# Optimization experiments

Hardware: AMD Instinct MI355X
Metric: run time of the kernel (lower is better)

## Reference

```python
import jax, jax.numpy as jnp
import numpy as np
import math


def _build_lookup(S):
    # Vectorized port of build_hierarchical_index_lookup_table (static, numpy).
    L = int(math.log2(S))
    total = 2 * S - 1
    max_valid = total - 2  # root is never a neighbor
    idx = np.full((S, L), -1, dtype=np.int32)
    cmask = np.zeros((S, L), dtype=bool)
    n = np.arange(S, dtype=np.int64)
    for lvl in range(L):
        if lvl == 0:
            nn = n ^ 1
            pair = n
        else:
            pair = n // 2 + S
            nn = pair ^ 1
        valid = nn <= max_valid
        idx[:, lvl] = np.where(valid, nn.astype(np.int32), idx[:, lvl])
        cmask[:, lvl] = np.where(valid, (pair < nn) & valid, cmask[:, lvl])
        n = nn
    return jnp.asarray(idx), jnp.asarray(cmask)


def _tree_kv(k, v, levels, scale):
    # Build parent nodes bottom-up. Parent K is the mean of its two children;
    # parent V is refined by the fused parent-self attention (build_parent_nodes):
    # 3-way softmax over [self, child0, child1] with eps 1e-9 in the denominator.
    K_parts, V_parts = [k], [v]
    Kc, Vc = k, v
    for _ in range(levels):
        Kc0, Kc1 = Kc[:, 0::2], Kc[:, 1::2]
        Vc0, Vc1 = Vc[:, 0::2], Vc[:, 1::2]
        Kp = 0.5 * (Kc0 + Kc1)
        Vp = 0.5 * (Vc0 + Vc1)
        s_self = jnp.einsum('bphd,bphd->bph', Kp, Kp) * scale
        s0 = jnp.einsum('bphd,bphd->bph', Kp, Kc0) * scale
        s1 = jnp.einsum('bphd,bphd->bph', Kp, Kc1) * scale
        m = jnp.maximum(s_self, jnp.maximum(s0, s1))
        e_self = jnp.exp(s_self - m)
        e0 = jnp.exp(s0 - m)
        e1 = jnp.exp(s1 - m)
        denom = e_self + e0 + e1 + 1e-9
        Vp = (e_self[..., None] * Vp + e0[..., None] * Vc0 + e1[..., None] * Vc1) / denom[..., None]
        K_parts.append(Kp)
        V_parts.append(Vp)
        Kc, Vc = Kp, Vp
    # Full tree: leaves first, then each parent level -> [B, 2S-1, H, D]
    return jnp.concatenate(K_parts, axis=1), jnp.concatenate(V_parts, axis=1)


def setup_inputs() -> dict:
    key = jax.random.key(0)
    kq, kk, kv = jax.random.split(key, 3)
    B, S, H, D = 4, 4096, 8, 64
    q = jax.random.normal(kq, (B, S, H, D), dtype=jnp.float32)
    k = jax.random.normal(kk, (B, S, H, D), dtype=jnp.float32)
    v = jax.random.normal(kv, (B, S, H, D), dtype=jnp.float32)
    return {'q': q, 'k': k, 'v': v}


def reference(q, k, v):
    B, S, H, D = q.shape
    L = int(math.log2(S))
    scale = 1.0 / math.sqrt(D)
    idx, cmask = _build_lookup(S)          # [S, L] int32, [S, L] bool
    Kf, Vf = _tree_kv(k, v, L, scale)      # [B, 2S-1, H, D]
    kc = Kf[:, idx]                        # [B, S, L, H, D] tree-indexed gather
    vc = Vf[:, idx]
    s_self = jnp.einsum('bshd,bshd->bsh', q, k) * scale
    s_cross = jnp.einsum('bshd,bslhd->bshl', q, kc) * scale
    s_cross = jnp.where(cmask[None, :, None, :], -jnp.inf, s_cross)
    m = jnp.maximum(s_self, jnp.max(s_cross, axis=-1))  # online-softmax max
    e_self = jnp.exp(s_self - m)
    e_cross = jnp.exp(s_cross - m[..., None])
    denom = e_self + jnp.sum(e_cross, axis=-1)
    out = (e_self[..., None] * v + jnp.einsum('bshl,bslhd->bshd', e_cross, vc)) / denom[..., None]
    return out
```

## Files before the change

kernel.cpp:

```cpp
#include <hip/hip_runtime.h>


#define S 4096
#define H 8
#define D 64
#define B 4
#define NBH 32
#define NHI 254
#define SCALE 0.125f
#define ROWF 68

__device__ inline float red16(float x) {
    x += __shfl_xor(x, 1);
    x += __shfl_xor(x, 2);
    x += __shfl_xor(x, 4);
    x += __shfl_xor(x, 8);
    return x;
}

__device__ inline float dot4(const float4 a, const float4 b) {
    return a.x * b.x + a.y * b.y + a.z * b.z + a.w * b.w;
}

__device__ inline float4 shfl_xor4(const float4 x, int m) {
    float4 r;
    r.x = __shfl_xor(x.x, m);
    r.y = __shfl_xor(x.y, m);
    r.z = __shfl_xor(x.z, m);
    r.w = __shfl_xor(x.w, m);
    return r;
}

__device__ inline float4 sel4(bool c, const float4 a, const float4 b) {
    float4 r;
    r.x = c ? a.x : b.x;
    r.y = c ? a.y : b.y;
    r.z = c ? a.z : b.z;
    r.w = c ? a.w : b.w;
    return r;
}

__device__ inline void combine(const float4 k0, const float4 k1,
                               const float4 v0, const float4 v1,
                               float4& kp, float4& vp) {
    kp.x = 0.5f * (k0.x + k1.x);
    kp.y = 0.5f * (k0.y + k1.y);
    kp.z = 0.5f * (k0.z + k1.z);
    kp.w = 0.5f * (k0.w + k1.w);
    float pss = red16(dot4(kp, kp)) * SCALE;
    float p0  = red16(dot4(kp, k0)) * SCALE;
    float p1  = red16(dot4(kp, k1)) * SCALE;
    float m  = fmaxf(pss, fmaxf(p0, p1));
    float es = __expf(pss - m), e0 = __expf(p0 - m), e1 = __expf(p1 - m);
    float inv = 1.0f / (es + e0 + e1 + 1e-9f);
    float h = 0.5f * es;
    vp.x = ((h + e0) * v0.x + (h + e1) * v1.x) * inv;
    vp.y = ((h + e0) * v0.y + (h + e1) * v1.y) * inv;
    vp.z = ((h + e0) * v0.z + (h + e1) * v1.z) * inv;
    vp.w = ((h + e0) * v0.w + (h + e1) * v1.w) * inv;
}

__global__ __launch_bounds__(256, 6) void chunk5(
    const float* __restrict__ k, const float* __restrict__ v,
    float* __restrict__ khi, float* __restrict__ vhi)
{
    __shared__ float l4k[4 * ROWF], l4v[4 * ROWF];
    const int t = threadIdx.x;
    const int sub = t & 15;
    const int pg = t >> 4;
    const int blk = blockIdx.x;
    const int pair = blk & 63;
    const int bh = blk >> 6;
    const int b = bh >> 3, h = bh & 7;
    const int csel = pg >> 3;
    const int jg = pg & 7;
    const int c = pair * 2 + csel;

    const int s0 = c * 32 + 4 * jg;
    const size_t a0 = ((((size_t)b * S + s0) * H + h) * D) + sub * 4;
    float4 kA = *(const float4*)(k + a0);
    float4 kB = *(const float4*)(k + a0 + H * D);
    float4 kC = *(const float4*)(k + a0 + 2 * H * D);
    float4 kD = *(const float4*)(k + a0 + 3 * H * D);
    float4 vA = *(const float4*)(v + a0);
    float4 vB = *(const float4*)(v + a0 + H * D);
    float4 vC = *(const float4*)(v + a0 + 2 * H * D);
    float4 vD = *(const float4*)(v + a0 + 3 * H * D);

    float4 k1a, v1a, k1b, v1b, k2, v2;
    combine(kA, kB, vA, vB, k1a, v1a);
    combine(kC, kD, vC, vD, k1b, v1b);
    combine(k1a, k1b, v1a, v1b, k2, v2);

    float4 p2k = shfl_xor4(k2, 16), p2v = shfl_xor4(v2, 16);
    float4 k3, v3;
    combine(sel4(jg & 1, p2k, k2), sel4(jg & 1, k2, p2k),
            sel4(jg & 1, p2v, v2), sel4(jg & 1, v2, p2v), k3, v3);

    float4 p3k = shfl_xor4(k3, 32), p3v = shfl_xor4(v3, 32);
    float4 k4, v4;
    combine(sel4(jg & 2, p3k, k3), sel4(jg & 2, k3, p3k),
            sel4(jg & 2, p3v, v3), sel4(jg & 2, v3, p3v), k4, v4);

    if ((jg & 3) == 0) {
        int row = csel * 2 + (jg >> 2);
        *(float4*)(l4k + row * ROWF + sub * 4) = k4;
        *(float4*)(l4v + row * ROWF + sub * 4) = v4;
    }
    __syncthreads();
    if (jg == 0) {
        int r0 = csel * 2, r1 = csel * 2 + 1;
        float4 ka4 = *(const float4*)(l4k + r0 * ROWF + sub * 4);
        float4 kb4 = *(const float4*)(l4k + r1 * ROWF + sub * 4);
        float4 va4 = *(const float4*)(l4v + r0 * ROWF + sub * 4);
        float4 vb4 = *(const float4*)(l4v + r1 * ROWF + sub * 4);
        float4 kp, vp;
        combine(ka4, kb4, va4, vb4, kp, vp);
        size_t g = ((size_t)bh * NHI + c) * 64 + sub * 4;
        *(float4*)(khi + g) = kp;
        *(float4*)(vhi + g) = vp;
    }
}

__global__ __launch_bounds__(256) void build_hi_half(
    float* __restrict__ khi, float* __restrict__ vhi)
{
    __shared__ float lk[64 * ROWF], lv[64 * ROWF];
    const int t = threadIdx.x;
    const int sub = t & 15;
    const int pg = t >> 4;
    const int bh = blockIdx.x >> 1;
    const int half = blockIdx.x & 1;
    size_t base = (size_t)bh * NHI * 64;
    const int rootO = half * 64;

    for (int i = t; i < 1024; i += 256) {
        int row = i >> 4, s16 = i & 15;
        *(float4*)(lk + row * ROWF + s16 * 4) =
            *(const float4*)(khi + base + (size_t)(rootO + row) * 64 + s16 * 4);
        *(float4*)(lv + row * ROWF + s16 * 4) =
            *(const float4*)(vhi + base + (size_t)(rootO + row) * 64 + s16 * 4);
    }
    __syncthreads();

#pragma unroll
    for (int tt = 1; tt <= 6; ++tt) {
        int nodes = 64 >> tt;
        int off = 256 - (256 >> tt);
        for (int j = pg; j < nodes; j += 16) {
            int r0 = (2 * j) << (tt - 1);
            int r1 = (2 * j + 1) << (tt - 1);
            float4 k0 = *(const float4*)(lk + r0 * ROWF + sub * 4);
            float4 k1 = *(const float4*)(lk + r1 * ROWF + sub * 4);
            float4 v0 = *(const float4*)(lv + r0 * ROWF + sub * 4);
            float4 v1 = *(const float4*)(lv + r1 * ROWF + sub * 4);
            float4 kp, vp;
            combine(k0, k1, v0, v1, kp, vp);
            *(float4*)(lk + (j << tt) * ROWF + sub * 4) = kp;
            *(float4*)(lv + (j << tt) * ROWF + sub * 4) = vp;
            size_t g = base + (size_t)(off + half * nodes + j) * 64 + sub * 4;
            *(float4*)(khi + g) = kp;
            *(float4*)(vhi + g) = vp;
        }
        __syncthreads();
    }
}

__global__ __launch_bounds__(256, 8) void attn32(
    const float* __restrict__ q, const float* __restrict__ k,
    const float* __restrict__ v,
    const float* __restrict__ khi, const float* __restrict__ vhi,
    float* __restrict__ out)
{
    __shared__ float tk[30 * ROWF], tv[30 * ROWF];
    __shared__ float pk[7 * ROWF], pv[7 * ROWF];
    const int t = threadIdx.x;
    const int sub = t & 15;
    const int pg = t >> 4;
    const int blk = blockIdx.x;
    const int c32 = blk & 127;
    const int bh = blk >> 7;
    const int b = bh >> 3, h = bh & 7;

    {
        int pl = (pg < 7) ? pg : pg - 8;
        if (pl >= 0 && pl < 7 && pg != 7 && pg != 15) {
            if ((c32 >> pl) & 1) {
                int off = 256 - (256 >> pl);
                int node = off + ((c32 >> pl) ^ 1);
                size_t a = ((size_t)bh * NHI + node) * 64 + sub * 4;
                if (pg < 7) *(float4*)(pk + pl * ROWF + sub * 4) = *(const float4*)(khi + a);
                else        *(float4*)(pv + pl * ROWF + sub * 4) = *(const float4*)(vhi + a);
            }
        }
    }

    const int s0 = c32 * 32 + 2 * pg;
    const size_t a0 = ((((size_t)b * S + s0) * H + h) * D) + sub * 4;
    const float4 k0 = *(const float4*)(k + a0);
    const float4 k1 = *(const float4*)(k + a0 + H * D);
    const float4 v0 = *(const float4*)(v + a0);
    const float4 v1 = *(const float4*)(v + a0 + H * D);
    const float4 q0 = *(const float4*)(q + a0);
    const float4 q1 = *(const float4*)(q + a0 + H * D);

    {
        float4 kp, vp;
        combine(k0, k1, v0, v1, kp, vp);
        *(float4*)(tk + pg * ROWF + sub * 4) = kp;
        *(float4*)(tv + pg * ROWF + sub * 4) = vp;
    }
    __syncthreads();

    if (pg < 8) {
        float4 ka = *(const float4*)(tk + (2 * pg) * ROWF + sub * 4);
        float4 kb = *(const float4*)(tk + (2 * pg + 1) * ROWF + sub * 4);
        float4 va = *(const float4*)(tv + (2 * pg) * ROWF + sub * 4);
        float4 vb = *(const float4*)(tv + (2 * pg + 1) * ROWF + sub * 4);
        float4 kp, vp;
        combine(ka, kb, va, vb, kp, vp);
        *(float4*)(tk + (16 + pg) * ROWF + sub * 4) = kp;
        *(float4*)(tv + (16 + pg) * ROWF + sub * 4) = vp;
    }
    __syncthreads();

    if (pg < 4) {
        float4 ka = *(const float4*)(tk + (16 + 2 * pg) * ROWF + sub * 4);
        float4 kb = *(const float4*)(tk + (16 + 2 * pg + 1) * ROWF + sub * 4);
        float4 va = *(const float4*)(tv + (16 + 2 * pg) * ROWF + sub * 4);
        float4 vb = *(const float4*)(tv + (16 + 2 * pg + 1) * ROWF + sub * 4);
        float4 kp, vp;
        combine(ka, kb, va, vb, kp, vp);
        *(float4*)(tk + (24 + pg) * ROWF + sub * 4) = kp;
        *(float4*)(tv + (24 + pg) * ROWF + sub * 4) = vp;
    }
    __syncthreads();

    if (pg < 2) {
        float4 ka = *(const float4*)(tk + (24 + 2 * pg) * ROWF + sub * 4);
        float4 kb = *(const float4*)(tk + (24 + 2 * pg + 1) * ROWF + sub * 4);
        float4 va = *(const float4*)(tv + (24 + 2 * pg) * ROWF + sub * 4);
        float4 vb = *(const float4*)(tv + (24 + 2 * pg + 1) * ROWF + sub * 4);
        float4 kp, vp;
        combine(ka, kb, va, vb, kp, vp);
        *(float4*)(tk + (28 + pg) * ROWF + sub * 4) = kp;
        *(float4*)(tv + (28 + pg) * ROWF + sub * 4) = vp;
    }
    __syncthreads();

#pragma unroll
    for (int r = 0; r < 2; ++r) {
        const int s = s0 + r;
        const float4 q4 = r ? q1 : q0;
        const float4 k4 = r ? k1 : k0;
        const float4 v4 = r ? v1 : v0;

        float ss = red16(dot4(q4, k4)) * SCALE;

        float sc[12];
        if (r) sc[0] = red16(dot4(q4, k0)) * SCALE;
        else   sc[0] = -1e38f;
#pragma unroll
        for (int l = 1; l <= 4; ++l) {
            if ((s >> l) & 1) {
                int base = 32 - (32 >> (l - 1));
                int loc = base + (((s >> l) ^ 1) - (c32 << (5 - l)));
                float4 kc = *(const float4*)(tk + loc * ROWF + sub * 4);
                sc[l] = red16(dot4(q4, kc)) * SCALE;
            } else sc[l] = -1e38f;
        }
#pragma unroll
        for (int l = 5; l <= 11; ++l) {
            if ((c32 >> (l - 5)) & 1) {
                float4 kc = *(const float4*)(pk + (l - 5) * ROWF + sub * 4);
                sc[l] = red16(dot4(q4, kc)) * SCALE;
            } else sc[l] = -1e38f;
        }

        float m = ss;
#pragma unroll
        for (int l = 0; l < 12; ++l) m = fmaxf(m, sc[l]);

        float es = __expf(ss - m);
        float denom = es;
        float4 acc;
        acc.x = es * v4.x; acc.y = es * v4.y;
        acc.z = es * v4.z; acc.w = es * v4.w;

        if (r) {
            float e = __expf(sc[0] - m);
            denom += e;
            acc.x += e * v0.x; acc.y += e * v0.y;
            acc.z += e * v0.z; acc.w += e * v0.w;
        }
#pragma unroll
        for (int l = 1; l <= 4; ++l) {
            if ((s >> l) & 1) {
                int base = 32 - (32 >> (l - 1));
                int loc = base + (((s >> l) ^ 1) - (c32 << (5 - l)));
                float4 vc = *(const float4*)(tv + loc * ROWF + sub * 4);
                float e = __expf(sc[l] - m);
                denom += e;
                acc.x += e * vc.x; acc.y += e * vc.y;
                acc.z += e * vc.z; acc.w += e * vc.w;
            }
        }
#pragma unroll
        for (int l = 5; l <= 11; ++l) {
            if ((c32 >> (l - 5)) & 1) {
                float4 vc = *(const float4*)(pv + (l - 5) * ROWF + sub * 4);
                float e = __expf(sc[l] - m);
                denom += e;
                acc.x += e * vc.x; acc.y += e * vc.y;
                acc.z += e * vc.z; acc.w += e * vc.w;
            }
        }
        float inv = 1.0f / denom;
        float4 o;
        o.x = acc.x * inv; o.y = acc.y * inv;
        o.z = acc.z * inv; o.w = acc.w * inv;
        *(float4*)(out + a0 + r * H * D) = o;
    }
}

extern "C" void kernel_launch(void* const* d_in, const int* in_sizes, int n_in,
                              void* d_out, int out_size, void* d_ws, size_t ws_size,
                              hipStream_t stream) {
    const float* q = (const float*)d_in[0];
    const float* k = (const float*)d_in[1];
    const float* v = (const float*)d_in[2];
    float* outp = (float*)d_out;
    float* khi = (float*)d_ws;
    float* vhi = khi + (size_t)NBH * NHI * D;

    hipLaunchKernelGGL(chunk5, dim3(NBH * 64), dim3(256), 0, stream,
                       k, v, khi, vhi);
    hipLaunchKernelGGL(build_hi_half, dim3(NBH * 2), dim3(256), 0, stream,
                       khi, vhi);
    hipLaunchKernelGGL(attn32, dim3(NBH * 128), dim3(256), 0, stream,
                       q, k, v, khi, vhi, outp);
}
```

Measured before the change: 157.4 us.

## Batch score reductions with a transposing butterfly across 16 lanes

Rewrites the attention phase so each lane accumulates partial dot products for all 16 candidate scores into a register array, then reduces them with a transposing butterfly. After it, each lane holds one full score, where before every score needed its own 4-step shuffle reduction. Max, exp and denominator are then computed lane-parallel, and weights are broadcast with shuffles for the V accumulation. Leaf-level dot products are interleaved with the tree-build phases, and launch bounds drop from 8 to 6 waves to allow more registers. The risk is higher register pressure from the two 16-float arrays and lower occupancy.

New measurement: 149.7 us. 1.05x faster.

```diff
diff --git a/kernel.cpp b/kernel.cpp
--- a/kernel.cpp
+++ b/kernel.cpp
@@ -38,6 +38,37 @@
     r.z = c ? a.z : b.z;
     r.w = c ? a.w : b.w;
     return r;
+}
+
+__device__ inline float bfly16(float* p, int sub) {
+    int b = (sub >> 3) & 1;
+#pragma unroll
+    for (int j = 0; j < 8; ++j) {
+        float mine = b ? p[j + 8] : p[j];
+        float send = b ? p[j] : p[j + 8];
+        p[j] = mine + __shfl_xor(send, 8);
+    }
+    b = (sub >> 2) & 1;
+#pragma unroll
+    for (int j = 0; j < 4; ++j) {
+        float mine = b ? p[j + 4] : p[j];
+        float send = b ? p[j] : p[j + 4];
+        p[j] = mine + __shfl_xor(send, 4);
+    }
+    b = (sub >> 1) & 1;
+#pragma unroll
+    for (int j = 0; j < 2; ++j) {
+        float mine = b ? p[j + 2] : p[j];
+        float send = b ? p[j] : p[j + 2];
+        p[j] = mine + __shfl_xor(send, 2);
+    }
+    b = sub & 1;
+    {
+        float mine = b ? p[1] : p[0];
+        float send = b ? p[0] : p[1];
+        p[0] = mine + __shfl_xor(send, 1);
+    }
+    return p[0];
 }
 
 __device__ inline void combine(const float4 k0, const float4 k1,
@@ -166,7 +197,7 @@
     }
 }
 
-__global__ __launch_bounds__(256, 8) void attn32(
+__global__ __launch_bounds__(256, 6) void attn32(
     const float* __restrict__ q, const float* __restrict__ k,
     const float* __restrict__ v,
     const float* __restrict__ khi, const float* __restrict__ vhi,
@@ -204,6 +235,13 @@
     const float4 q0 = *(const float4*)(q + a0);
     const float4 q1 = *(const float4*)(q + a0 + H * D);
 
+    float p0[16], p1[16];
+#pragma unroll
+    for (int j = 0; j < 16; ++j) { p0[j] = 0.0f; p1[j] = 0.0f; }
+    p0[0] = dot4(q0, k0);
+    p1[0] = dot4(q1, k1);
+    p1[1] = dot4(q1, k0);
+
     {
         float4 kp, vp;
         combine(k0, k1, v0, v1, kp, vp);
@@ -212,6 +250,11 @@
     }
     __syncthreads();
 
+    if (pg & 1) {
+        float4 kc = *(const float4*)(tk + (pg ^ 1) * ROWF + sub * 4);
+        p0[2] = dot4(q0, kc);
+        p1[2] = dot4(q1, kc);
+    }
     if (pg < 8) {
         float4 ka = *(const float4*)(tk + (2 * pg) * ROWF + sub * 4);
         float4 kb = *(const float4*)(tk + (2 * pg + 1) * ROWF + sub * 4);
@@ -224,6 +267,11 @@
     }
     __syncthreads();
 
+    if ((pg >> 1) & 1) {
+        float4 kc = *(const float4*)(tk + (16 + ((pg >> 1) ^ 1)) * ROWF + sub * 4);
+        p0[3] = dot4(q0, kc);
+        p1[3] = dot4(q1, kc);
+    }
     if (pg < 4) {
         float4 ka = *(const float4*)(tk + (16 + 2 * pg) * ROWF + sub * 4);
         float4 kb = *(const float4*)(tk + (16 + 2 * pg + 1) * ROWF + sub * 4);
@@ -236,6 +284,11 @@
     }
     __syncthreads();
 
+    if ((pg >> 2) & 1) {
+        float4 kc = *(const float4*)(tk + (24 + ((pg >> 2) ^ 1)) * ROWF + sub * 4);
+        p0[4] = dot4(q0, kc);
+        p1[4] = dot4(q1, kc);
+    }
     if (pg < 2) {
         float4 ka = *(const float4*)(tk + (24 + 2 * pg) * ROWF + sub * 4);
         float4 kb = *(const float4*)(tk + (24 + 2 * pg + 1) * ROWF + sub * 4);
@@ -248,79 +301,91 @@
     }
     __syncthreads();
 
-#pragma unroll
-    for (int r = 0; r < 2; ++r) {
-        const int s = s0 + r;
-        const float4 q4 = r ? q1 : q0;
-        const float4 k4 = r ? k1 : k0;
-        const float4 v4 = r ? v1 : v0;
-
-        float ss = red16(dot4(q4, k4)) * SCALE;
-
-        float sc[12];
-        if (r) sc[0] = red16(dot4(q4, k0)) * SCALE;
-        else   sc[0] = -1e38f;
-#pragma unroll
-        for (int l = 1; l <= 4; ++l) {
-            if ((s >> l) & 1) {
-                int base = 32 - (32 >> (l - 1));
-                int loc = base + (((s >> l) ^ 1) - (c32 << (5 - l)));
-                float4 kc = *(const float4*)(tk + loc * ROWF + sub * 4);
-                sc[l] = red16(dot4(q4, kc)) * SCALE;
-            } else sc[l] = -1e38f;
+    if ((pg >> 3) & 1) {
+        float4 kc = *(const float4*)(tk + (28 + ((pg >> 3) ^ 1)) * ROWF + sub * 4);
+        p0[5] = dot4(q0, kc);
+        p1[5] = dot4(q1, kc);
+    }
+#pragma unroll
+    for (int l = 5; l <= 11; ++l) {
+        if ((c32 >> (l - 5)) & 1) {
+            float4 kc = *(const float4*)(pk + (l - 5) * ROWF + sub * 4);
+            p0[l + 1] = dot4(q0, kc);
+            p1[l + 1] = dot4(q1, kc);
         }
-#pragma unroll
-        for (int l = 5; l <= 11; ++l) {
-            if ((c32 >> (l - 5)) & 1) {
-                float4 kc = *(const float4*)(pk + (l - 5) * ROWF + sub * 4);
-                sc[l] = red16(dot4(q4, kc)) * SCALE;
-            } else sc[l] = -1e38f;
+    }
+
+    float sc0 = bfly16(p0, sub) * SCALE;
+    float sc1 = bfly16(p1, sub) * SCALE;
+
+    const bool vcom =
+        (sub == 0) ||
+        (sub >= 2 && sub <= 5 && ((pg >> (sub - 2)) & 1)) ||
+        (sub >= 6 && sub <= 12 && ((c32 >> (sub - 6)) & 1));
+    const bool ok0 = vcom;
+    const bool ok1 = vcom || (sub == 1);
+
+    float xm0 = ok0 ? sc0 : -1e38f;
+    float xm1 = ok1 ? sc1 : -1e38f;
+    xm0 = fmaxf(xm0, __shfl_xor(xm0, 1)); xm1 = fmaxf(xm1, __shfl_xor(xm1, 1));
+    xm0 = fmaxf(xm0, __shfl_xor(xm0, 2)); xm1 = fmaxf(xm1, __shfl_xor(xm1, 2));
+    xm0 = fmaxf(xm0, __shfl_xor(xm0, 4)); xm1 = fmaxf(xm1, __shfl_xor(xm1, 4));
+    xm0 = fmaxf(xm0, __shfl_xor(xm0, 8)); xm1 = fmaxf(xm1, __shfl_xor(xm1, 8));
+
+    float e0 = ok0 ? __expf(sc0 - xm0) : 0.0f;
+    float e1 = ok1 ? __expf(sc1 - xm1) : 0.0f;
+    float d0 = red16(e0);
+    float d1 = red16(e1);
+
+    float4 acc0, acc1;
+    {
+        float w0 = __shfl(e0, 0, 16);
+        float w1 = __shfl(e1, 0, 16);
+        acc0.x = w0 * v0.x; acc0.y = w0 * v0.y;
+        acc0.z = w0 * v0.z; acc0.w = w0 * v0.w;
+        acc1.x = w1 * v1.x; acc1.y = w1 * v1.y;
+        acc1.z = w1 * v1.z; acc1.w = w1 * v1.w;
+        float wl = __shfl(e1, 1, 16);
+        acc1.x += wl * v0.x; acc1.y += wl * v0.y;
+        acc1.z += wl * v0.z; acc1.w += wl * v0.w;
+    }
+#pragma unroll
+    for (int l = 1; l <= 4; ++l) {
+        if ((pg >> (l - 1)) & 1) {
+            int loc = (l == 1) ? (pg ^ 1)
+                    : (l == 2) ? (16 + ((pg >> 1) ^ 1))
+                    : (l == 3) ? (24 + ((pg >> 2) ^ 1))
+                               : (28 + ((pg >> 3) ^ 1));
+            float4 vc = *(const float4*)(tv + loc * ROWF + sub * 4);
+            float w0 = __shfl(e0, l + 1, 16);
+            float w1 = __shfl(e1, l + 1, 16);
+            acc0.x += w0 * vc.x; acc0.y += w0 * vc.y;
+            acc0.z += w0 * vc.z; acc0.w += w0 * vc.w;
+            acc1.x += w1 * vc.x; acc1.y += w1 * vc.y;
+            acc1.z += w1 * vc.z; acc1.w += w1 * vc.w;
         }
-
-        float m = ss;
-#pragma unroll
-        for (int l = 0; l < 12; ++l) m = fmaxf(m, sc[l]);
-
-        float es = __expf(ss - m);
-        float denom = es;
-        float4 acc;
-        acc.x = es * v4.x; acc.y = es * v4.y;
-        acc.z = es * v4.z; acc.w = es * v4.w;
-
-        if (r) {
-            float e = __expf(sc[0] - m);
-            denom += e;
-            acc.x += e * v0.x; acc.y += e * v0.y;
-            acc.z += e * v0.z; acc.w += e * v0.w;
+    }
+#pragma unroll
+    for (int l = 5; l <= 11; ++l) {
+        if ((c32 >> (l - 5)) & 1) {
+            float4 vc = *(const float4*)(pv + (l - 5) * ROWF + sub * 4);
+            float w0 = __shfl(e0, l + 1, 16);
+            float w1 = __shfl(e1, l + 1, 16);
+            acc0.x += w0 * vc.x; acc0.y += w0 * vc.y;
+            acc0.z += w0 * vc.z; acc0.w += w0 * vc.w;
+            acc1.x += w1 * vc.x; acc1.y += w1 * vc.y;
+            acc1.z += w1 * vc.z; acc1.w += w1 * vc.w;
         }
-#pragma unroll
-        for (int l = 1; l <= 4; ++l) {
-            if ((s >> l) & 1) {
-                int base = 32 - (32 >> (l - 1));
-                int loc = base + (((s >> l) ^ 1) - (c32 << (5 - l)));
-                float4 vc = *(const float4*)(tv + loc * ROWF + sub * 4);
-                float e = __expf(sc[l] - m);
-                denom += e;
-                acc.x += e * vc.x; acc.y += e * vc.y;
-                acc.z += e * vc.z; acc.w += e * vc.w;
-            }
-        }
-#pragma unroll
-        for (int l = 5; l <= 11; ++l) {
-            if ((c32 >> (l - 5)) & 1) {
-                float4 vc = *(const float4*)(pv + (l - 5) * ROWF + sub * 4);
-                float e = __expf(sc[l] - m);
-                denom += e;
-                acc.x += e * vc.x; acc.y += e * vc.y;
-                acc.z += e * vc.z; acc.w += e * vc.w;
-            }
-        }
-        float inv = 1.0f / denom;
-        float4 o;
-        o.x = acc.x * inv; o.y = acc.y * inv;
-        o.z = acc.z * inv; o.w = acc.w * inv;
-        *(float4*)(out + a0 + r * H * D) = o;
-    }
+    }
+
+    float i0 = 1.0f / d0, i1 = 1.0f / d1;
+    float4 o0, o1;
+    o0.x = acc0.x * i0; o0.y = acc0.y * i0;
+    o0.z = acc0.z * i0; o0.w = acc0.w * i0;
+    o1.x = acc1.x * i1; o1.y = acc1.y * i1;
+    o1.z = acc1.z * i1; o1.w = acc1.w * i1;
+    *(float4*)(out + a0) = o0;
+    *(float4*)(out + a0 + H * D) = o1;
 }
 
 extern "C" void kernel_launch(void* const* d_in, const int* in_sizes, int n_in,
```
